# Kernel optimization log

Hardware: AMD Instinct MI355X
Metric: run time of the kernel (lower is better)

## Reference

```python
import jax, jax.numpy as jnp
import numpy as np
import math

B, S, H, D = 2, 2048, 12, 64
DROPOUT_P = 0.1

def setup_inputs() -> dict:
    rng = jax.random.key(0)
    kq, kk, kv = jax.random.split(rng, 3)
    query = jax.random.normal(kq, (B, S, H, D), dtype=jnp.float32)
    key = jax.random.normal(kk, (B, S, H, D), dtype=jnp.float32)
    value = jax.random.normal(kv, (B, S, H, D), dtype=jnp.float32)
    return {"query": query, "key": key, "value": value}

def reference(query, key, value):
    # [B,S,H,D] -> [B,H,S,D]
    q = jnp.transpose(query, (0, 2, 1, 3))
    k = jnp.transpose(key, (0, 2, 1, 3))
    v = jnp.transpose(value, (0, 2, 1, 3))
    q = q / math.sqrt(q.shape[-1])
    # scores in fp32 (explicit cast in original)
    scores = jnp.einsum('bhsd,bhtd->bhst', q, k).astype(jnp.float32)
    attn = jax.nn.softmax(scores, axis=-1)
    # dropout (training mode in original); deterministic mask with fixed key
    keep = jax.random.bernoulli(jax.random.key(42), 1.0 - DROPOUT_P, attn.shape)
    attn = jnp.where(keep, attn / (1.0 - DROPOUT_P), 0.0)
    # explicit fp16 cast of attention weights before AV matmul
    attn = attn.astype(jnp.float16)
    out = jnp.einsum('bhst,bhtd->bhsd', attn, v)  # promotes to fp32 (v is fp32)
    return out
```

## Files before the change

### kernel.cpp

```cpp
#include <hip/hip_runtime.h>
#include <stdint.h>

#define B_ 2
#define S_ 2048
#define H_ 12
#define D_ 64
#define HD_ (H_ * D_)
#define KEEP_HI 3865470464u
#define C_INIT 0.15200309344504997f
#define QSCALE 0.18033688011112042f

typedef __attribute__((ext_vector_type(8))) _Float16 f16x8;
typedef __attribute__((ext_vector_type(4))) _Float16 f16x4;
typedef __attribute__((ext_vector_type(4))) float f32x4;

#define MFMA32 __builtin_amdgcn_mfma_f32_16x16x32_f16
#define MFMA16 __builtin_amdgcn_mfma_f32_16x16x16f16

__device__ __forceinline__ uint32_t tf_bits(uint32_t i) {
    const uint32_t k1 = 42u, k2 = 0x1BD11BF0u;
    uint32_t x0 = 0u, x1 = i + k1;
#define TF_R(r) { x0 += x1; x1 = __builtin_rotateleft32(x1, (r)); x1 ^= x0; }
    TF_R(13) TF_R(15) TF_R(26) TF_R(6)
    x0 += k1; x1 += k2 + 1u;
    TF_R(17) TF_R(29) TF_R(16) TF_R(24)
    x0 += k2; x1 += 2u;
    TF_R(13) TF_R(15) TF_R(26) TF_R(6)
    x1 += k1 + 3u;
    TF_R(17) TF_R(29) TF_R(16) TF_R(24)
    x0 += k1; x1 += k2 + 4u;
    TF_R(13) TF_R(15) TF_R(26) TF_R(6)
    x0 += k2; x1 += 5u;
#undef TF_R
    return x0 ^ x1;
}

template<int HALVES>
__global__ __launch_bounds__(256, 4)
void attn_kernel(const float* __restrict__ Q, const float* __restrict__ K,
                 const float* __restrict__ V, float* __restrict__ O,
                 float* __restrict__ W) {
    constexpr int NT = 32 / HALVES;
    __shared__ __align__(16) _Float16 Kh[64][72];
    __shared__ __align__(16) _Float16 Vh[64][72];

    const int tid  = threadIdx.x;
    const int lane = tid & 63;
    const int wid  = tid >> 6;
    const int g    = lane >> 4;
    const int sl   = lane & 15;

    const int bid  = blockIdx.x;
    const int half = bid / 768;
    const int bid2 = bid % 768;
    const int qb = bid2 & 31;
    const int bh = bid2 >> 5;
    const int h  = bh % H_;
    const int b  = bh / H_;
    const int kt0 = half * NT;

    const int s = qb * 64 + wid * 16 + sl;
    const size_t kvbase = (size_t)b * S_ * HD_ + (size_t)h * D_;

    f16x8 qh[2], ql[2];
    {
        const float* qp = Q + ((size_t)(b * S_ + s) * H_ + h) * D_;
#pragma unroll
        for (int ks = 0; ks < 2; ++ks) {
            int d0 = 32 * ks + 8 * g;
            float4 f0 = *reinterpret_cast<const float4*>(qp + d0);
            float4 f1 = *reinterpret_cast<const float4*>(qp + d0 + 4);
            float ff[8] = {f0.x, f0.y, f0.z, f0.w, f1.x, f1.y, f1.z, f1.w};
#pragma unroll
            for (int j = 0; j < 8; ++j) {
                float f = ff[j] * QSCALE;
                _Float16 hi = (_Float16)f;
                qh[ks][j] = hi;
                ql[ks][j] = (_Float16)(f - (float)hi);
            }
        }
    }

    const int ktK = tid >> 2;
    const int kd0 = (tid & 3) * 16;
    const int vdd = (tid & 31) * 2;
    const int vt0 = (tid >> 5) * 8;

    float4 kreg0, kreg1, kreg2, kreg3;
    float2 vreg[8];

#define LOADTILE(ktg_) do {                                                         \
        const float* kp = K + kvbase + (size_t)((ktg_) * 64 + ktK) * HD_ + kd0;     \
        kreg0 = *reinterpret_cast<const float4*>(kp);                               \
        kreg1 = *reinterpret_cast<const float4*>(kp + 4);                           \
        kreg2 = *reinterpret_cast<const float4*>(kp + 8);                           \
        kreg3 = *reinterpret_cast<const float4*>(kp + 12);                          \
        const float* vp = V + kvbase + (size_t)((ktg_) * 64 + vt0) * HD_ + vdd;     \
        _Pragma("unroll")                                                           \
        for (int j = 0; j < 8; ++j) vreg[j] = *reinterpret_cast<const float2*>(vp + j * HD_); \
    } while (0)

    LOADTILE(kt0);

    float lrun = 0.f;
    f32x4 outacc[4];
#pragma unroll
    for (int m = 0; m < 4; ++m) outacc[m] = (f32x4){0.f, 0.f, 0.f, 0.f};

    const uint32_t rowbase = ((uint32_t)(bh * S_ + s)) << 11;

    for (int ktl = 0; ktl < NT; ++ktl) {
        const int ktg = kt0 + ktl;
        if (ktl) __syncthreads();
        {
            float ff[16] = {kreg0.x, kreg0.y, kreg0.z, kreg0.w,
                            kreg1.x, kreg1.y, kreg1.z, kreg1.w,
                            kreg2.x, kreg2.y, kreg2.z, kreg2.w,
                            kreg3.x, kreg3.y, kreg3.z, kreg3.w};
            f16x8 h0, h1;
#pragma unroll
            for (int j = 0; j < 8; ++j) { h0[j] = (_Float16)ff[j]; h1[j] = (_Float16)ff[8 + j]; }
            *reinterpret_cast<f16x8*>(&Kh[ktK][kd0])     = h0;
            *reinterpret_cast<f16x8*>(&Kh[ktK][kd0 + 8]) = h1;
            f16x8 v0, v1;
#pragma unroll
            for (int j = 0; j < 8; ++j) { v0[j] = (_Float16)vreg[j].x; v1[j] = (_Float16)vreg[j].y; }
            *reinterpret_cast<f16x8*>(&Vh[vdd][vt0])     = v0;
            *reinterpret_cast<f16x8*>(&Vh[vdd + 1][vt0]) = v1;
        }
        __syncthreads();
        if (ktl + 1 < NT) LOADTILE(ktg + 1);

        f32x4 sc[4];
#pragma unroll
        for (int m = 0; m < 4; ++m) sc[m] = (f32x4){C_INIT, C_INIT, C_INIT, C_INIT};
#pragma unroll
        for (int m = 0; m < 4; ++m) {
#pragma unroll
            for (int ks = 0; ks < 2; ++ks) {
                f16x8 ah = *reinterpret_cast<const f16x8*>(&Kh[16 * m + sl][8 * g + 32 * ks]);
                sc[m] = MFMA32(ah, qh[ks], sc[m], 0, 0, 0);
                sc[m] = MFMA32(ah, ql[ks], sc[m], 0, 0, 0);
            }
        }

        const uint32_t fb = rowbase + (uint32_t)(ktg * 64);
#pragma unroll
        for (int m = 0; m < 4; ++m) {
            int t0 = 16 * m + 4 * g;
            f16x4 w;
#pragma unroll
            for (int r = 0; r < 4; ++r) {
                float e = exp2f(sc[m][r]);
                lrun += e;
                uint32_t bits = tf_bits(fb + (uint32_t)(t0 + r));
                float pf = (bits < KEEP_HI) ? e : 0.0f;
                w[r] = (_Float16)pf;
            }
#pragma unroll
            for (int md = 0; md < 4; ++md) {
                f16x4 va = *reinterpret_cast<const f16x4*>(&Vh[16 * md + sl][16 * m + 4 * g]);
                outacc[md] = MFMA16(va, w, outacc[md], 0, 0, 0);
            }
        }
    }
#undef LOADTILE

    lrun += __shfl_xor(lrun, 16);
    lrun += __shfl_xor(lrun, 32);

    if (HALVES == 1) {
        const float invL = 1.0f / (0.9f * lrun);
        float* op = O + ((size_t)bh * S_ + s) * D_;
#pragma unroll
        for (int m = 0; m < 4; ++m) {
            int dd0 = 16 * m + 4 * g;
            float4 f = make_float4(outacc[m][0] * invL, outacc[m][1] * invL,
                                   outacc[m][2] * invL, outacc[m][3] * invL);
            *reinterpret_cast<float4*>(op + dd0) = f;
        }
    } else {
        float* wp = W + ((size_t)(half * 24 + bh) * S_ + s) * 68;
#pragma unroll
        for (int m = 0; m < 4; ++m) {
            int dd0 = 16 * m + 4 * g;
            float4 f = make_float4(outacc[m][0], outacc[m][1], outacc[m][2], outacc[m][3]);
            *reinterpret_cast<float4*>(wp + dd0) = f;
        }
        if (g == 0) wp[64] = lrun;
    }
}

__global__ __launch_bounds__(256)
void combine_kernel(const float* __restrict__ W, float* __restrict__ O) {
    const int row = blockIdx.x * 4 + (threadIdx.x >> 6);
    const int dd  = threadIdx.x & 63;
    const float* w0 = W + (size_t)row * 68;
    const float* w1 = W + ((size_t)(24 * 2048) + row) * 68;
    const float L = w0[64] + w1[64];
    const float scale = 1.0f / (0.9f * L);
    O[(size_t)row * 64 + dd] = (w0[dd] + w1[dd]) * scale;
}

extern "C" void kernel_launch(void* const* d_in, const int* in_sizes, int n_in,
                              void* d_out, int out_size, void* d_ws, size_t ws_size,
                              hipStream_t stream) {
    const float* Q = (const float*)d_in[0];
    const float* K = (const float*)d_in[1];
    const float* V = (const float*)d_in[2];
    float* O = (float*)d_out;
    (void)in_sizes; (void)n_in; (void)out_size;

    const size_t ws_need = (size_t)2 * 24 * 2048 * 68 * sizeof(float);
    if (d_ws && ws_size >= ws_need) {
        float* W = (float*)d_ws;
        attn_kernel<2><<<dim3(1536), dim3(256), 0, stream>>>(Q, K, V, O, W);
        combine_kernel<<<dim3(24 * 2048 / 4), dim3(256), 0, stream>>>(W, O);
    } else {
        attn_kernel<1><<<dim3(768), dim3(256), 0, stream>>>(Q, K, V, O, nullptr);
    }
}
```

Measured before the change: 234.4 us.

## Double-buffer K/V shared tiles with XOR swizzle and one barrier per tile

Replaces the single padded K/V LDS tiles with two swizzled buffers. The loop is unrolled by two so the next tile is converted and written into the alternate buffer while the current one is consumed, which halves the number of barriers per tile. The XOR swizzle replaces row padding to avoid LDS bank conflicts. In exchange it doubles LDS use, which may limit occupancy, and the unrolled body adds register pressure.

New measurement: 261.5 us. +11.6%, slower.

```diff
diff --git a/kernel.cpp b/kernel.cpp
--- a/kernel.cpp
+++ b/kernel.cpp
@@ -5,7 +5,7 @@
 #define S_ 2048
 #define H_ 12
 #define D_ 64
-#define HD_ (H_ * D_)
+#define HD_ 768
 #define KEEP_HI 3865470464u
 #define C_INIT 0.15200309344504997f
 #define QSCALE 0.18033688011112042f
@@ -35,14 +35,19 @@
     return x0 ^ x1;
 }
 
+__device__ __forceinline__ uint32_t swz_off(int row, int col) {
+    uint32_t byte = (((uint32_t)row) << 7) + (((uint32_t)col) << 1);
+    return byte ^ (((uint32_t)(row & 7)) << 4);
+}
+
 template<int HALVES>
 __global__ __launch_bounds__(256, 4)
 void attn_kernel(const float* __restrict__ Q, const float* __restrict__ K,
                  const float* __restrict__ V, float* __restrict__ O,
                  float* __restrict__ W) {
     constexpr int NT = 32 / HALVES;
-    __shared__ __align__(16) _Float16 Kh[64][72];
-    __shared__ __align__(16) _Float16 Vh[64][72];
+    __shared__ __align__(16) _Float16 KT[2][64 * 64];
+    __shared__ __align__(16) _Float16 VT[2][64 * 64];
 
     const int tid  = threadIdx.x;
     const int lane = tid & 63;
@@ -100,7 +105,58 @@
         for (int j = 0; j < 8; ++j) vreg[j] = *reinterpret_cast<const float2*>(vp + j * HD_); \
     } while (0)
 
-    LOADTILE(kt0);
+#define CVTWRITE(P) do {                                                            \
+        float ff[16] = {kreg0.x, kreg0.y, kreg0.z, kreg0.w,                         \
+                        kreg1.x, kreg1.y, kreg1.z, kreg1.w,                         \
+                        kreg2.x, kreg2.y, kreg2.z, kreg2.w,                         \
+                        kreg3.x, kreg3.y, kreg3.z, kreg3.w};                        \
+        f16x8 h0, h1;                                                               \
+        _Pragma("unroll")                                                           \
+        for (int j = 0; j < 8; ++j) { h0[j] = (_Float16)ff[j]; h1[j] = (_Float16)ff[8 + j]; } \
+        *reinterpret_cast<f16x8*>((char*)KT[P] + swz_off(ktK, kd0))     = h0;       \
+        *reinterpret_cast<f16x8*>((char*)KT[P] + swz_off(ktK, kd0 + 8)) = h1;       \
+        f16x8 v0, v1;                                                               \
+        _Pragma("unroll")                                                           \
+        for (int j = 0; j < 8; ++j) { v0[j] = (_Float16)vreg[j].x; v1[j] = (_Float16)vreg[j].y; } \
+        *reinterpret_cast<f16x8*>((char*)VT[P] + swz_off(vdd, vt0))     = v0;       \
+        *reinterpret_cast<f16x8*>((char*)VT[P] + swz_off(vdd + 1, vt0)) = v1;       \
+    } while (0)
+
+#define COMPUTE(P, ktg_) do {                                                       \
+        f32x4 sc[4];                                                                \
+        _Pragma("unroll")                                                           \
+        for (int m = 0; m < 4; ++m) sc[m] = (f32x4){C_INIT, C_INIT, C_INIT, C_INIT}; \
+        _Pragma("unroll")                                                           \
+        for (int m = 0; m < 4; ++m) {                                               \
+            _Pragma("unroll")                                                       \
+            for (int ks = 0; ks < 2; ++ks) {                                        \
+                f16x8 ah = *reinterpret_cast<const f16x8*>(                         \
+                    (const char*)KT[P] + swz_off(16 * m + sl, 8 * g + 32 * ks));    \
+                sc[m] = MFMA32(ah, qh[ks], sc[m], 0, 0, 0);                         \
+                sc[m] = MFMA32(ah, ql[ks], sc[m], 0, 0, 0);                         \
+            }                                                                       \
+        }                                                                           \
+        const uint32_t fb = rowbase + (uint32_t)((ktg_) * 64);                      \
+        _Pragma("unroll")                                                           \
+        for (int m = 0; m < 4; ++m) {                                               \
+            int t0 = 16 * m + 4 * g;                                                \
+            f16x4 w;                                                                \
+            _Pragma("unroll")                                                       \
+            for (int r = 0; r < 4; ++r) {                                           \
+                float e = exp2f(sc[m][r]);                    \
+                lrun += e;                                                          \
+                uint32_t bits = tf_bits(fb + (uint32_t)(t0 + r));                   \
+                float pf = (bits < KEEP_HI) ? e : 0.0f;                             \
+                w[r] = (_Float16)pf;                    \
+            }                                                                       \
+            _Pragma("unroll")                                                       \
+            for (int md = 0; md < 4; ++md) {                                        \
+                f16x4 va = *reinterpret_cast<const f16x4*>(                         \
+                    (const char*)VT[P] + swz_off(16 * md + sl, 16 * m + 4 * g));    \
+                outacc[md] = MFMA16(va, w, outacc[md], 0, 0, 0);                    \
+            }                                                                       \
+        }                                                                           \
+    } while (0)
 
     float lrun = 0.f;
     f32x4 outacc[4];
@@ -109,62 +165,23 @@
 
     const uint32_t rowbase = ((uint32_t)(bh * S_ + s)) << 11;
 
-    for (int ktl = 0; ktl < NT; ++ktl) {
+    LOADTILE(kt0);
+    CVTWRITE(0);
+
+    for (int ktl = 0; ktl < NT; ktl += 2) {
         const int ktg = kt0 + ktl;
-        if (ktl) __syncthreads();
-        {
-            float ff[16] = {kreg0.x, kreg0.y, kreg0.z, kreg0.w,
-                            kreg1.x, kreg1.y, kreg1.z, kreg1.w,
-                            kreg2.x, kreg2.y, kreg2.z, kreg2.w,
-                            kreg3.x, kreg3.y, kreg3.z, kreg3.w};
-            f16x8 h0, h1;
-#pragma unroll
-            for (int j = 0; j < 8; ++j) { h0[j] = (_Float16)ff[j]; h1[j] = (_Float16)ff[8 + j]; }
-            *reinterpret_cast<f16x8*>(&Kh[ktK][kd0])     = h0;
-            *reinterpret_cast<f16x8*>(&Kh[ktK][kd0 + 8]) = h1;
-            f16x8 v0, v1;
-#pragma unroll
-            for (int j = 0; j < 8; ++j) { v0[j] = (_Float16)vreg[j].x; v1[j] = (_Float16)vreg[j].y; }
-            *reinterpret_cast<f16x8*>(&Vh[vdd][vt0])     = v0;
-            *reinterpret_cast<f16x8*>(&Vh[vdd + 1][vt0]) = v1;
-        }
         __syncthreads();
-        if (ktl + 1 < NT) LOADTILE(ktg + 1);
-
-        f32x4 sc[4];
-#pragma unroll
-        for (int m = 0; m < 4; ++m) sc[m] = (f32x4){C_INIT, C_INIT, C_INIT, C_INIT};
-#pragma unroll
-        for (int m = 0; m < 4; ++m) {
-#pragma unroll
-            for (int ks = 0; ks < 2; ++ks) {
-                f16x8 ah = *reinterpret_cast<const f16x8*>(&Kh[16 * m + sl][8 * g + 32 * ks]);
-                sc[m] = MFMA32(ah, qh[ks], sc[m], 0, 0, 0);
-                sc[m] = MFMA32(ah, ql[ks], sc[m], 0, 0, 0);
-            }
-        }
-
-        const uint32_t fb = rowbase + (uint32_t)(ktg * 64);
-#pragma unroll
-        for (int m = 0; m < 4; ++m) {
-            int t0 = 16 * m + 4 * g;
-            f16x4 w;
-#pragma unroll
-            for (int r = 0; r < 4; ++r) {
-                float e = exp2f(sc[m][r]);
-                lrun += e;
-                uint32_t bits = tf_bits(fb + (uint32_t)(t0 + r));
-                float pf = (bits < KEEP_HI) ? e : 0.0f;
-                w[r] = (_Float16)pf;
-            }
-#pragma unroll
-            for (int md = 0; md < 4; ++md) {
-                f16x4 va = *reinterpret_cast<const f16x4*>(&Vh[16 * md + sl][16 * m + 4 * g]);
-                outacc[md] = MFMA16(va, w, outacc[md], 0, 0, 0);
-            }
-        }
+        LOADTILE(ktg + 1);
+        COMPUTE(0, ktg);
+        CVTWRITE(1);
+        __syncthreads();
+        if (ktl + 2 < NT) LOADTILE(ktg + 2);
+        COMPUTE(1, ktg + 1);
+        if (ktl + 2 < NT) CVTWRITE(0);
     }
 #undef LOADTILE
+#undef CVTWRITE
+#undef COMPUTE
 
     lrun += __shfl_xor(lrun, 16);
     lrun += __shfl_xor(lrun, 32);
```

## Drop shared-memory K/V staging; load K/V directly from global per wave

Applied to the files above, without the earlier changes.

Removes the LDS tiles, block barriers and the register prefetch pipeline. Each wave now reads its K and V fragments straight from global memory and converts them to fp16 in registers. For the PV product the MFMA operands are swapped (weights as A, V as B), which changes the output layout and the store indexing; the row sum for normalization is fetched with a shuffle. This removes synchronisation and LDS traffic, but each of the four waves in a block now loads K/V separately, using scalar strided loads for V, so it leans on cache hits and adds global load latency with no prefetch.

After: 325.6 us. +38.9%, slower.

```diff
diff --git a/kernel.cpp b/kernel.cpp
--- a/kernel.cpp
+++ b/kernel.cpp
@@ -5,7 +5,7 @@
 #define S_ 2048
 #define H_ 12
 #define D_ 64
-#define HD_ (H_ * D_)
+#define HD_ 768
 #define KEEP_HI 3865470464u
 #define C_INIT 0.15200309344504997f
 #define QSCALE 0.18033688011112042f
@@ -41,25 +41,22 @@
                  const float* __restrict__ V, float* __restrict__ O,
                  float* __restrict__ W) {
     constexpr int NT = 32 / HALVES;
-    __shared__ __align__(16) _Float16 Kh[64][72];
-    __shared__ __align__(16) _Float16 Vh[64][72];
-
     const int tid  = threadIdx.x;
     const int lane = tid & 63;
-    const int wid  = tid >> 6;
     const int g    = lane >> 4;
     const int sl   = lane & 15;
 
-    const int bid  = blockIdx.x;
-    const int half = bid / 768;
-    const int bid2 = bid % 768;
-    const int qb = bid2 & 31;
-    const int bh = bid2 >> 5;
-    const int h  = bh % H_;
-    const int b  = bh / H_;
-    const int kt0 = half * NT;
+    const int gw   = blockIdx.x * 4 + (tid >> 6);
+    const int half = (HALVES == 2) ? (gw / 3072) : 0;
+    const int rem  = (HALVES == 2) ? (gw % 3072) : gw;
+    const int bh   = rem >> 7;
+    const int sg   = rem & 127;
+    const int h    = bh % H_;
+    const int b    = bh / H_;
+    const int sbase = sg * 16;
+    const int s    = sbase + sl;
+    const int kt0  = half * NT;
 
-    const int s = qb * 64 + wid * 16 + sl;
     const size_t kvbase = (size_t)b * S_ * HD_ + (size_t)h * D_;
 
     f16x8 qh[2], ql[2];
@@ -81,113 +78,88 @@
         }
     }
 
-    const int ktK = tid >> 2;
-    const int kd0 = (tid & 3) * 16;
-    const int vdd = (tid & 31) * 2;
-    const int vt0 = (tid >> 5) * 8;
-
-    float4 kreg0, kreg1, kreg2, kreg3;
-    float2 vreg[8];
-
-#define LOADTILE(ktg_) do {                                                         \
-        const float* kp = K + kvbase + (size_t)((ktg_) * 64 + ktK) * HD_ + kd0;     \
-        kreg0 = *reinterpret_cast<const float4*>(kp);                               \
-        kreg1 = *reinterpret_cast<const float4*>(kp + 4);                           \
-        kreg2 = *reinterpret_cast<const float4*>(kp + 8);                           \
-        kreg3 = *reinterpret_cast<const float4*>(kp + 12);                          \
-        const float* vp = V + kvbase + (size_t)((ktg_) * 64 + vt0) * HD_ + vdd;     \
-        _Pragma("unroll")                                                           \
-        for (int j = 0; j < 8; ++j) vreg[j] = *reinterpret_cast<const float2*>(vp + j * HD_); \
-    } while (0)
-
-    LOADTILE(kt0);
-
     float lrun = 0.f;
     f32x4 outacc[4];
 #pragma unroll
-    for (int m = 0; m < 4; ++m) outacc[m] = (f32x4){0.f, 0.f, 0.f, 0.f};
+    for (int nb = 0; nb < 4; ++nb) outacc[nb] = (f32x4){0.f, 0.f, 0.f, 0.f};
 
     const uint32_t rowbase = ((uint32_t)(bh * S_ + s)) << 11;
 
     for (int ktl = 0; ktl < NT; ++ktl) {
         const int ktg = kt0 + ktl;
-        if (ktl) __syncthreads();
-        {
-            float ff[16] = {kreg0.x, kreg0.y, kreg0.z, kreg0.w,
-                            kreg1.x, kreg1.y, kreg1.z, kreg1.w,
-                            kreg2.x, kreg2.y, kreg2.z, kreg2.w,
-                            kreg3.x, kreg3.y, kreg3.z, kreg3.w};
-            f16x8 h0, h1;
-#pragma unroll
-            for (int j = 0; j < 8; ++j) { h0[j] = (_Float16)ff[j]; h1[j] = (_Float16)ff[8 + j]; }
-            *reinterpret_cast<f16x8*>(&Kh[ktK][kd0])     = h0;
-            *reinterpret_cast<f16x8*>(&Kh[ktK][kd0 + 8]) = h1;
-            f16x8 v0, v1;
-#pragma unroll
-            for (int j = 0; j < 8; ++j) { v0[j] = (_Float16)vreg[j].x; v1[j] = (_Float16)vreg[j].y; }
-            *reinterpret_cast<f16x8*>(&Vh[vdd][vt0])     = v0;
-            *reinterpret_cast<f16x8*>(&Vh[vdd + 1][vt0]) = v1;
-        }
-        __syncthreads();
-        if (ktl + 1 < NT) LOADTILE(ktg + 1);
+        const float* kb = K + kvbase + (size_t)(ktg * 64) * HD_;
+        const float* vb = V + kvbase + (size_t)(ktg * 64) * HD_;
 
         f32x4 sc[4];
 #pragma unroll
         for (int m = 0; m < 4; ++m) sc[m] = (f32x4){C_INIT, C_INIT, C_INIT, C_INIT};
 #pragma unroll
         for (int m = 0; m < 4; ++m) {
+            const float* kp = kb + (16 * m + sl) * HD_ + 8 * g;
 #pragma unroll
             for (int ks = 0; ks < 2; ++ks) {
-                f16x8 ah = *reinterpret_cast<const f16x8*>(&Kh[16 * m + sl][8 * g + 32 * ks]);
+                float4 a0 = *reinterpret_cast<const float4*>(kp + 32 * ks);
+                float4 a1 = *reinterpret_cast<const float4*>(kp + 32 * ks + 4);
+                f16x8 ah;
+                ah[0] = (_Float16)a0.x; ah[1] = (_Float16)a0.y;
+                ah[2] = (_Float16)a0.z; ah[3] = (_Float16)a0.w;
+                ah[4] = (_Float16)a1.x; ah[5] = (_Float16)a1.y;
+                ah[6] = (_Float16)a1.z; ah[7] = (_Float16)a1.w;
                 sc[m] = MFMA32(ah, qh[ks], sc[m], 0, 0, 0);
                 sc[m] = MFMA32(ah, ql[ks], sc[m], 0, 0, 0);
             }
         }
 
         const uint32_t fb = rowbase + (uint32_t)(ktg * 64);
+        f16x4 w[4];
 #pragma unroll
         for (int m = 0; m < 4; ++m) {
             int t0 = 16 * m + 4 * g;
-            f16x4 w;
 #pragma unroll
             for (int r = 0; r < 4; ++r) {
                 float e = exp2f(sc[m][r]);
                 lrun += e;
                 uint32_t bits = tf_bits(fb + (uint32_t)(t0 + r));
                 float pf = (bits < KEEP_HI) ? e : 0.0f;
-                w[r] = (_Float16)pf;
+                w[m][r] = (_Float16)pf;
             }
+        }
+
 #pragma unroll
-            for (int md = 0; md < 4; ++md) {
-                f16x4 va = *reinterpret_cast<const f16x4*>(&Vh[16 * md + sl][16 * m + 4 * g]);
-                outacc[md] = MFMA16(va, w, outacc[md], 0, 0, 0);
+        for (int m = 0; m < 4; ++m) {
+            const float* vrow = vb + (16 * m + 4 * g) * HD_ + sl;
+#pragma unroll
+            for (int nb = 0; nb < 4; ++nb) {
+                f16x4 vf;
+#pragma unroll
+                for (int r = 0; r < 4; ++r)
+                    vf[r] = (_Float16)vrow[r * HD_ + 16 * nb];
+                outacc[nb] = MFMA16(w[m], vf, outacc[nb], 0, 0, 0);
             }
         }
     }
-#undef LOADTILE
 
     lrun += __shfl_xor(lrun, 16);
     lrun += __shfl_xor(lrun, 32);
 
     if (HALVES == 1) {
-        const float invL = 1.0f / (0.9f * lrun);
-        float* op = O + ((size_t)bh * S_ + s) * D_;
+        float* ob = O + ((size_t)bh * S_ + sbase) * D_;
 #pragma unroll
-        for (int m = 0; m < 4; ++m) {
-            int dd0 = 16 * m + 4 * g;
-            float4 f = make_float4(outacc[m][0] * invL, outacc[m][1] * invL,
-                                   outacc[m][2] * invL, outacc[m][3] * invL);
-            *reinterpret_cast<float4*>(op + dd0) = f;
+        for (int jj = 0; jj < 4; ++jj) {
+            float invL = 1.0f / (0.9f * __shfl(lrun, 4 * g + jj));
+#pragma unroll
+            for (int nb = 0; nb < 4; ++nb)
+                ob[(size_t)(4 * g + jj) * D_ + 16 * nb + sl] = outacc[nb][jj] * invL;
         }
     } else {
-        float* wp = W + ((size_t)(half * 24 + bh) * S_ + s) * 68;
+        float* wbase = W + ((size_t)(half * 24 + bh) * S_ + sbase) * 68;
 #pragma unroll
-        for (int m = 0; m < 4; ++m) {
-            int dd0 = 16 * m + 4 * g;
-            float4 f = make_float4(outacc[m][0], outacc[m][1], outacc[m][2], outacc[m][3]);
-            *reinterpret_cast<float4*>(wp + dd0) = f;
+        for (int jj = 0; jj < 4; ++jj) {
+#pragma unroll
+            for (int nb = 0; nb < 4; ++nb)
+                wbase[(4 * g + jj) * 68 + 16 * nb + sl] = outacc[nb][jj];
         }
-        if (g == 0) wp[64] = lrun;
+        if (g == 0) wbase[sl * 68 + 64] = lrun;
     }
 }
 
```

## Precompute dropout mask as bitmask in separate kernel

Applied to the files above, without the earlier changes.

Adds a mask kernel that evaluates the Threefry dropout bits once per element and packs them into 64-bit ballots in workspace. The attention kernel then reads one 64-bit word per key tile instead of running the hash inline. The rotate is also expressed via the alignbit intrinsic. This moves the hash cost out of the MFMA-bound loop, which may let it overlap less with MFMA, in exchange for an extra launch and about 12.6 MB of mask writes and reads.

Result: slower. 336.6 us (+43.6%).

```diff
diff --git a/kernel.cpp b/kernel.cpp
--- a/kernel.cpp
+++ b/kernel.cpp
@@ -5,10 +5,11 @@
 #define S_ 2048
 #define H_ 12
 #define D_ 64
-#define HD_ (H_ * D_)
+#define HD_ 768
 #define KEEP_HI 3865470464u
 #define C_INIT 0.15200309344504997f
 #define QSCALE 0.18033688011112042f
+#define NCHUNK 1572864u
 
 typedef __attribute__((ext_vector_type(8))) _Float16 f16x8;
 typedef __attribute__((ext_vector_type(4))) _Float16 f16x4;
@@ -17,10 +18,14 @@
 #define MFMA32 __builtin_amdgcn_mfma_f32_16x16x32_f16
 #define MFMA16 __builtin_amdgcn_mfma_f32_16x16x16f16
 
+__device__ __forceinline__ uint32_t rotl1(uint32_t x, int r) {
+    return __builtin_amdgcn_alignbit(x, x, 32 - r);
+}
+
 __device__ __forceinline__ uint32_t tf_bits(uint32_t i) {
     const uint32_t k1 = 42u, k2 = 0x1BD11BF0u;
     uint32_t x0 = 0u, x1 = i + k1;
-#define TF_R(r) { x0 += x1; x1 = __builtin_rotateleft32(x1, (r)); x1 ^= x0; }
+#define TF_R(r) { x0 += x1; x1 = rotl1(x1, (r)); x1 ^= x0; }
     TF_R(13) TF_R(15) TF_R(26) TF_R(6)
     x0 += k1; x1 += k2 + 1u;
     TF_R(17) TF_R(29) TF_R(16) TF_R(24)
@@ -35,11 +40,25 @@
     return x0 ^ x1;
 }
 
+__global__ __launch_bounds__(256, 8)
+void mask_kernel(uint64_t* __restrict__ M) {
+    const int lane = threadIdx.x & 63;
+    const uint32_t w = blockIdx.x * 4u + (threadIdx.x >> 6);
+    const uint32_t c0 = w * 192u;
+    uint32_t i = c0 * 64u + (uint32_t)lane;
+    for (uint32_t j = 0; j < 192u; ++j) {
+        uint32_t bits = tf_bits(i);
+        uint64_t bal = __ballot(bits < KEEP_HI);
+        if (lane == 0) M[c0 + j] = bal;
+        i += 64u;
+    }
+}
+
 template<int HALVES>
 __global__ __launch_bounds__(256, 4)
 void attn_kernel(const float* __restrict__ Q, const float* __restrict__ K,
                  const float* __restrict__ V, float* __restrict__ O,
-                 float* __restrict__ W) {
+                 float* __restrict__ W, const uint64_t* __restrict__ M) {
     constexpr int NT = 32 / HALVES;
     __shared__ __align__(16) _Float16 Kh[64][72];
     __shared__ __align__(16) _Float16 Vh[64][72];
@@ -61,6 +80,7 @@
 
     const int s = qb * 64 + wid * 16 + sl;
     const size_t kvbase = (size_t)b * S_ * HD_ + (size_t)h * D_;
+    const uint64_t* mrow = M + (size_t)(bh * S_ + s) * 32;
 
     f16x8 qh[2], ql[2];
     {
@@ -107,8 +127,6 @@
 #pragma unroll
     for (int m = 0; m < 4; ++m) outacc[m] = (f32x4){0.f, 0.f, 0.f, 0.f};
 
-    const uint32_t rowbase = ((uint32_t)(bh * S_ + s)) << 11;
-
     for (int ktl = 0; ktl < NT; ++ktl) {
         const int ktg = kt0 + ktl;
         if (ktl) __syncthreads();
@@ -129,6 +147,7 @@
             *reinterpret_cast<f16x8*>(&Vh[vdd + 1][vt0]) = v1;
         }
         __syncthreads();
+        const uint64_t bal = mrow[ktg];
         if (ktl + 1 < NT) LOADTILE(ktg + 1);
 
         f32x4 sc[4];
@@ -144,17 +163,16 @@
             }
         }
 
-        const uint32_t fb = rowbase + (uint32_t)(ktg * 64);
-#pragma unroll
-        for (int m = 0; m < 4; ++m) {
-            int t0 = 16 * m + 4 * g;
+        const uint64_t balg = bal >> (4 * g);
+#pragma unroll
+        for (int m = 0; m < 4; ++m) {
+            const uint32_t mb = (uint32_t)(balg >> (16 * m));
             f16x4 w;
 #pragma unroll
             for (int r = 0; r < 4; ++r) {
                 float e = exp2f(sc[m][r]);
                 lrun += e;
-                uint32_t bits = tf_bits(fb + (uint32_t)(t0 + r));
-                float pf = (bits < KEEP_HI) ? e : 0.0f;
+                float pf = ((mb >> r) & 1u) ? e : 0.0f;
                 w[r] = (_Float16)pf;
             }
 #pragma unroll
@@ -211,12 +229,17 @@
     float* O = (float*)d_out;
     (void)in_sizes; (void)n_in; (void)out_size;
 
-    const size_t ws_need = (size_t)2 * 24 * 2048 * 68 * sizeof(float);
-    if (d_ws && ws_size >= ws_need) {
-        float* W = (float*)d_ws;
-        attn_kernel<2><<<dim3(1536), dim3(256), 0, stream>>>(Q, K, V, O, W);
+    const size_t mask_bytes = (size_t)NCHUNK * 8u;
+    const size_t w_bytes    = (size_t)2 * 24 * 2048 * 68 * sizeof(float);
+
+    uint64_t* M = (uint64_t*)d_ws;
+    mask_kernel<<<dim3(2048), dim3(256), 0, stream>>>(M);
+
+    if (ws_size >= mask_bytes + w_bytes) {
+        float* W = (float*)((char*)d_ws + mask_bytes);
+        attn_kernel<2><<<dim3(1536), dim3(256), 0, stream>>>(Q, K, V, O, W, M);
         combine_kernel<<<dim3(24 * 2048 / 4), dim3(256), 0, stream>>>(W, O);
     } else {
-        attn_kernel<1><<<dim3(768), dim3(256), 0, stream>>>(Q, K, V, O, nullptr);
-    }
-}
+        attn_kernel<1><<<dim3(768), dim3(256), 0, stream>>>(Q, K, V, O, nullptr, M);
+    }
+}
```
